# Kernel optimization log

Hardware: AMD Instinct MI355X
Metric: run time of the kernel (lower is better)

## Reference

```python
import jax, jax.numpy as jnp
import numpy as np

N, DIN, H, NCLS = 1024, 128, 64, 40
NEG = -1e30  # stand-in for -inf in masked max (grad-safe)


def _linw(k, fan_in, fan_out):
    s = 1.0 / np.sqrt(fan_in)
    return jax.random.uniform(k, (fan_in, fan_out), jnp.float32, -s, s)


def setup_inputs() -> dict:
    key = jax.random.key(0)
    ks = jax.random.split(key, 10)
    x = jax.random.normal(ks[0], (N, DIN), jnp.float32)
    A = jax.random.bernoulli(ks[1], 0.05, (N, N))  # bool adjacency
    D2 = 2 * H  # layer output width (concat self || neigh)
    return {
        "x": x, "A": A,
        # layer 1 (in=DIN)
        "Wp1": _linw(ks[2], DIN, DIN), "bp1": jnp.zeros((DIN,), jnp.float32),
        "Ws1": _linw(ks[3], DIN, H),   "bs1": jnp.zeros((H,), jnp.float32),
        "Wn1": _linw(ks[4], DIN, H),   "bn1": jnp.zeros((H,), jnp.float32),
        # layer 2 (in=2*H)
        "Wp2": _linw(ks[5], D2, D2),   "bp2": jnp.zeros((D2,), jnp.float32),
        "Ws2": _linw(ks[6], D2, H),    "bs2": jnp.zeros((H,), jnp.float32),
        "Wn2": _linw(ks[7], D2, H),    "bn2": jnp.zeros((H,), jnp.float32),
        # head
        "Wh": _linw(ks[8], D2, NCLS),  "bh": jnp.zeros((NCLS,), jnp.float32),
    }


def _sage_layer(x, A, Wp, bp, Ws, bs, Wn, bn):
    # maxpool aggregator: relu(Linear_pool(x_u)), elementwise max over neighbors u of v
    pooled = jax.nn.relu(x @ Wp + bp)                                  # [N, Din]
    agg = jnp.max(jnp.where(A[:, :, None], pooled[None, :, :], NEG), axis=1)  # [N, Din]
    agg = jnp.where(agg <= NEG * 0.5, 0.0, agg)                        # isolated nodes -> 0
    # out_channels = 2*hidden: concat(self transform, neighbor transform)
    return jnp.concatenate([x @ Ws + bs, agg @ Wn + bn], axis=-1)      # [N, 2H]


def _block(x, A, Wp, bp, Ws, bs, Wn, bn):
    h = jax.nn.relu(_sage_layer(x, A, Wp, bp, Ws, bs, Wn, bn))
    nrm = jnp.maximum(jnp.linalg.norm(h, axis=-1, keepdims=True), 1e-12)
    return h / nrm


def reference(x, A, Wp1, bp1, Ws1, bs1, Wn1, bn1,
              Wp2, bp2, Ws2, bs2, Wn2, bn2, Wh, bh):
    h = _block(x, A, Wp1, bp1, Ws1, bs1, Wn1, bn1)
    h = _block(h, A, Wp2, bp2, Ws2, bs2, Wn2, bn2)
    return h @ Wh + bh  # [N, n_classes]
```

## Files before the change

kernel.cpp:

```cpp
#include <hip/hip_runtime.h>

#define NN 1024

__global__ __launch_bounds__(384) void lin_first(
    const float* __restrict__ X, const float* __restrict__ Wp,
    const float* __restrict__ bp, const float* __restrict__ Ws,
    const float* __restrict__ bs, float* __restrict__ pooled,
    float* __restrict__ sbuf)
{
    __shared__ float xL[4][128];
    __shared__ float lp[2][4][192];
    const int v0 = blockIdx.x * 4;
    const int tid = threadIdx.x;
    for (int i = tid; i < 512; i += 384) xL[i >> 7][i & 127] = X[v0 * 128 + i];
    __syncthreads();
    {
        const int kh = (tid >= 192) ? 1 : 0;
        const int j = tid - kh * 192;
        const float* w; int ld;
        if (j < 128) { w = Wp + j;         ld = 128; }
        else         { w = Ws + (j - 128); ld = 64;  }
        float a0 = 0.f, a1 = 0.f, a2 = 0.f, a3 = 0.f;
        const int k0 = kh * 64;
        #pragma unroll 4
        for (int k = 0; k < 64; ++k) {
            const float wv = w[(k0 + k) * ld];
            a0 += xL[0][k0 + k] * wv;  a1 += xL[1][k0 + k] * wv;
            a2 += xL[2][k0 + k] * wv;  a3 += xL[3][k0 + k] * wv;
        }
        lp[kh][0][j] = a0; lp[kh][1][j] = a1; lp[kh][2][j] = a2; lp[kh][3][j] = a3;
    }
    __syncthreads();
    if (tid < 192) {
        #pragma unroll
        for (int r = 0; r < 4; ++r) {
            const float t = lp[0][r][tid] + lp[1][r][tid];
            if (tid < 128) pooled[(v0 + r) * 128 + tid] = fmaxf(t + bp[tid], 0.f);
            else           sbuf[(v0 + r) * 64 + (tid - 128)] = t + bs[tid - 128];
        }
    }
}

template <int MODE>
__global__ __launch_bounds__(512) void agg_kernel(
    const int* __restrict__ A, const float* __restrict__ pooled,
    const float* __restrict__ sbuf,
    const float* __restrict__ Wn, const float* __restrict__ bn,
    const float* __restrict__ Wp2, const float* __restrict__ bp2,
    const float* __restrict__ Ws2, const float* __restrict__ bs2,
    float* __restrict__ out_pooled, float* __restrict__ out_s,
    float* __restrict__ outh)
{
    __shared__ unsigned long long masks[16];
    __shared__ int pfx[16];
    __shared__ int cntS;
    __shared__ int nbr[NN];
    __shared__ float part[4][128];
    __shared__ float aggL[128];
    __shared__ float wpart[4][64];
    __shared__ float hL[128];
    __shared__ float lpart[2][192];
    __shared__ float red[2];

    const int v    = blockIdx.x;
    const int tid  = threadIdx.x;
    const int lane = tid & 63;
    const int wv   = tid >> 6;

    const int* Arow = A + v * NN;
    #pragma unroll
    for (int i = 0; i < 2; ++i) {
        const int c = wv * 2 + i;
        const unsigned long long m = __ballot(Arow[c * 64 + lane] != 0);
        if (lane == 0) masks[c] = m;
    }
    __syncthreads();
    if (tid == 0) {
        int off = 0;
        #pragma unroll
        for (int c = 0; c < 16; ++c) { pfx[c] = off; off += __popcll(masks[c]); }
        cntS = off;
    }
    __syncthreads();
    #pragma unroll
    for (int i = 0; i < 2; ++i) {
        const int c = wv * 2 + i;
        const unsigned long long m = masks[c];
        if ((m >> lane) & 1ull) {
            const int pos = pfx[c] + __popcll(m & ((1ull << lane) - 1ull));
            nbr[pos] = c * 64 + lane;
        }
    }
    __syncthreads();
    const int n = cntS;

    const int d    = tid & 127;
    const int team = tid >> 7;
    float a0 = -1e30f, a1 = -1e30f, a2 = -1e30f, a3 = -1e30f;
    int p = team;
    for (; p + 12 < n; p += 16) {
        a0 = fmaxf(a0, pooled[nbr[p]      * 128 + d]);
        a1 = fmaxf(a1, pooled[nbr[p + 4]  * 128 + d]);
        a2 = fmaxf(a2, pooled[nbr[p + 8]  * 128 + d]);
        a3 = fmaxf(a3, pooled[nbr[p + 12] * 128 + d]);
    }
    for (; p < n; p += 4) a0 = fmaxf(a0, pooled[nbr[p] * 128 + d]);
    part[team][d] = fmaxf(fmaxf(a0, a1), fmaxf(a2, a3));
    __syncthreads();

    if (team == 0) {
        const float m = fmaxf(fmaxf(part[0][d], part[1][d]),
                              fmaxf(part[2][d], part[3][d]));
        aggL[d] = (m <= -5e29f) ? 0.f : m;
    }
    __syncthreads();

    if (d >= 64) {
        const int j = d - 64;
        const float* w = Wn + j;
        const int k0 = team * 32;
        float pv = 0.f;
        #pragma unroll 8
        for (int k = 0; k < 32; ++k) pv += aggL[k0 + k] * w[(k0 + k) * 64];
        wpart[team][j] = pv;
    }
    __syncthreads();

    float val = 0.f;
    if (tid < 128) {
        if (d < 64) val = sbuf[v * 64 + d];
        else {
            const int j = d - 64;
            val = bn[j] + wpart[0][j] + wpart[1][j] + wpart[2][j] + wpart[3][j];
        }
        val = fmaxf(val, 0.f);
        float ss = val * val;
        #pragma unroll
        for (int off = 32; off >= 1; off >>= 1) ss += __shfl_xor(ss, off, 64);
        if ((tid & 63) == 0) red[tid >> 6] = ss;
    }
    __syncthreads();
    if (tid < 128) {
        const float nrm = fmaxf(sqrtf(red[0] + red[1]), 1e-12f);
        hL[tid] = val / nrm;
    }
    __syncthreads();

    if (MODE == 0) {
        if (tid < 384) {
            const int kh = (tid >= 192) ? 1 : 0;
            const int j  = tid - kh * 192;
            const float* w; int ld;
            if (j < 128) { w = Wp2 + j;         ld = 128; }
            else         { w = Ws2 + (j - 128); ld = 64;  }
            float a = 0.f;
            const int k0 = kh * 64;
            #pragma unroll 4
            for (int k = 0; k < 64; ++k) a += hL[k0 + k] * w[(k0 + k) * ld];
            lpart[kh][j] = a;
        }
        __syncthreads();
        if (tid < 192) {
            const float r = lpart[0][tid] + lpart[1][tid];
            if (tid < 128) out_pooled[v * 128 + tid] = fmaxf(r + bp2[tid], 0.f);
            else           out_s[v * 64 + (tid - 128)] = r + bs2[tid - 128];
        }
    } else {
        if (tid < 64 || (tid >= 256 && tid < 320)) {
            const int kh = (tid >= 256) ? 1 : 0;
            const int j  = tid - kh * 256;
            if (j < 40) {
                float a = 0.f;
                const int k0 = kh * 64;
                #pragma unroll 4
                for (int k = 0; k < 64; ++k) a += hL[k0 + k] * Wp2[(k0 + k) * 40 + j];
                lpart[kh][j] = a;
            }
        }
        __syncthreads();
        if (tid < 40) outh[v * 40 + tid] = bp2[tid] + lpart[0][tid] + lpart[1][tid];
    }
}

extern "C" void kernel_launch(void* const* d_in, const int* in_sizes, int n_in,
                              void* d_out, int out_size, void* d_ws, size_t ws_size,
                              hipStream_t stream) {
    const float* x   = (const float*)d_in[0];
    const int*   A   = (const int*)  d_in[1];
    const float* Wp1 = (const float*)d_in[2];
    const float* bp1 = (const float*)d_in[3];
    const float* Ws1 = (const float*)d_in[4];
    const float* bs1 = (const float*)d_in[5];
    const float* Wn1 = (const float*)d_in[6];
    const float* bn1 = (const float*)d_in[7];
    const float* Wp2 = (const float*)d_in[8];
    const float* bp2 = (const float*)d_in[9];
    const float* Ws2 = (const float*)d_in[10];
    const float* bs2 = (const float*)d_in[11];
    const float* Wn2 = (const float*)d_in[12];
    const float* bn2 = (const float*)d_in[13];
    const float* Wh  = (const float*)d_in[14];
    const float* bh  = (const float*)d_in[15];
    float* out = (float*)d_out;

    char* ws = (char*)d_ws;
    float* pooled1 = (float*)(ws);
    float* s1      = (float*)(ws + (512u << 10));
    float* pooled2 = (float*)(ws + (768u << 10));
    float* s2      = (float*)(ws + (1280u << 10));

    lin_first<<<NN / 4, 384, 0, stream>>>(x, Wp1, bp1, Ws1, bs1, pooled1, s1);
    agg_kernel<0><<<NN, 512, 0, stream>>>(A, pooled1, s1, Wn1, bn1,
                                          Wp2, bp2, Ws2, bs2,
                                          pooled2, s2, nullptr);
    agg_kernel<1><<<NN, 512, 0, stream>>>(A, pooled2, s2, Wn2, bn2,
                                          Wh, bh, nullptr, nullptr,
                                          nullptr, nullptr, out);
}
```

Measured before the change: 28.85 us.

## Fuse three launches into one persistent kernel with grid-wide barriers

Replaces the three separate launches (first linear, two aggregation layers) with a single persistent kernel of 256 blocks, each handling 4 nodes, separated by software grid barriers built on atomics. The neighbor lists are built once per block and reused for both layers, and the self-transform results stay in shared memory instead of going through global buffers. The aim is to remove launch gaps and the duplicated adjacency scan. In exchange it depends on all 256 blocks being resident at once, adds barrier spin cost and a memset, and gives each block more serial work with less parallelism per node.

```diff
diff --git a/kernel.cpp b/kernel.cpp
--- a/kernel.cpp
+++ b/kernel.cpp
@@ -1,32 +1,67 @@
 #include <hip/hip_runtime.h>
 
-#define NN 1024
-
-__global__ __launch_bounds__(384) void lin_first(
-    const float* __restrict__ X, const float* __restrict__ Wp,
-    const float* __restrict__ bp, const float* __restrict__ Ws,
-    const float* __restrict__ bs, float* __restrict__ pooled,
-    float* __restrict__ sbuf)
-{
-    __shared__ float xL[4][128];
-    __shared__ float lp[2][4][192];
-    const int v0 = blockIdx.x * 4;
-    const int tid = threadIdx.x;
-    for (int i = tid; i < 512; i += 384) xL[i >> 7][i & 127] = X[v0 * 128 + i];
-    __syncthreads();
-    {
+#define NN   1024
+#define NBLK 256
+
+struct SharedState {
+    float xL[4][128];
+    float s1L[4][64];
+    float s2L[4][64];
+    float aggL[4][128];
+    float hL[4][128];
+    float lp[2][4][192];
+    float redL[4][2];
+    unsigned long long masksL[4][16];
+    int pfxL[4][16];
+    int cntL[4];
+    int nbrL[4][NN];
+};
+
+__device__ __forceinline__ void gbar(int* cnt, int* gen) {
+    __syncthreads();
+    if (threadIdx.x == 0) {
+        const int g = __hip_atomic_load(gen, __ATOMIC_RELAXED,
+                                        __HIP_MEMORY_SCOPE_AGENT);
+        __threadfence();
+        if (__hip_atomic_fetch_add(cnt, 1, __ATOMIC_ACQ_REL,
+                                   __HIP_MEMORY_SCOPE_AGENT) == NBLK - 1) {
+            __hip_atomic_store(cnt, 0, __ATOMIC_RELAXED,
+                               __HIP_MEMORY_SCOPE_AGENT);
+            __hip_atomic_fetch_add(gen, 1, __ATOMIC_RELEASE,
+                                   __HIP_MEMORY_SCOPE_AGENT);
+        } else {
+            int spins = 0;
+            while (__hip_atomic_load(gen, __ATOMIC_ACQUIRE,
+                                     __HIP_MEMORY_SCOPE_AGENT) == g) {
+                __builtin_amdgcn_s_sleep(1);
+                if (++spins > 10000000) break;
+            }
+        }
+        __threadfence();
+    }
+    __syncthreads();
+}
+
+__device__ __forceinline__ void lin_block(
+    const float (&in)[4][128],
+    const float* __restrict__ Wp, const float* __restrict__ bp,
+    const float* __restrict__ Ws, const float* __restrict__ bs,
+    float* __restrict__ pooledG, float (&sL)[4][64],
+    float (&lp)[2][4][192], int v0, int tid)
+{
+    if (tid < 384) {
         const int kh = (tid >= 192) ? 1 : 0;
         const int j = tid - kh * 192;
         const float* w; int ld;
         if (j < 128) { w = Wp + j;         ld = 128; }
         else         { w = Ws + (j - 128); ld = 64;  }
+        const int k0 = kh * 64;
         float a0 = 0.f, a1 = 0.f, a2 = 0.f, a3 = 0.f;
-        const int k0 = kh * 64;
         #pragma unroll 4
         for (int k = 0; k < 64; ++k) {
             const float wv = w[(k0 + k) * ld];
-            a0 += xL[0][k0 + k] * wv;  a1 += xL[1][k0 + k] * wv;
-            a2 += xL[2][k0 + k] * wv;  a3 += xL[3][k0 + k] * wv;
+            a0 += in[0][k0 + k] * wv;  a1 += in[1][k0 + k] * wv;
+            a2 += in[2][k0 + k] * wv;  a3 += in[3][k0 + k] * wv;
         }
         lp[kh][0][j] = a0; lp[kh][1][j] = a1; lp[kh][2][j] = a2; lp[kh][3][j] = a3;
     }
@@ -35,150 +70,151 @@
         #pragma unroll
         for (int r = 0; r < 4; ++r) {
             const float t = lp[0][r][tid] + lp[1][r][tid];
-            if (tid < 128) pooled[(v0 + r) * 128 + tid] = fmaxf(t + bp[tid], 0.f);
-            else           sbuf[(v0 + r) * 64 + (tid - 128)] = t + bs[tid - 128];
-        }
-    }
-}
-
-template <int MODE>
-__global__ __launch_bounds__(512) void agg_kernel(
-    const int* __restrict__ A, const float* __restrict__ pooled,
-    const float* __restrict__ sbuf,
+            if (tid < 128) pooledG[(v0 + r) * 128 + tid] = fmaxf(t + bp[tid], 0.f);
+            else           sL[r][tid - 128] = t + bs[tid - 128];
+        }
+    }
+    __syncthreads();
+}
+
+__device__ __forceinline__ void gather_rows(
+    const float* __restrict__ src, const int (&nbrL)[4][NN],
+    const int (&cntL)[4], float (&aggL)[4][128], int tid)
+{
+    const int d = tid & 127, r = tid >> 7;
+    const int n = cntL[r];
+    const int* nb = nbrL[r];
+    float a0 = -1e30f, a1 = -1e30f, a2 = -1e30f, a3 = -1e30f;
+    int p = 0;
+    for (; p + 3 < n; p += 4) {
+        a0 = fmaxf(a0, src[nb[p]     * 128 + d]);
+        a1 = fmaxf(a1, src[nb[p + 1] * 128 + d]);
+        a2 = fmaxf(a2, src[nb[p + 2] * 128 + d]);
+        a3 = fmaxf(a3, src[nb[p + 3] * 128 + d]);
+    }
+    for (; p < n; ++p) a0 = fmaxf(a0, src[nb[p] * 128 + d]);
+    const float m = fmaxf(fmaxf(a0, a1), fmaxf(a2, a3));
+    aggL[r][d] = (m <= -5e29f) ? 0.f : m;
+    __syncthreads();
+}
+
+__device__ __forceinline__ void wn_norm(
     const float* __restrict__ Wn, const float* __restrict__ bn,
+    const float (&aggL)[4][128], const float (&sL)[4][64],
+    float (&lp)[2][4][192], float (&redL)[4][2], float (&hL)[4][128],
+    int tid)
+{
+    {
+        const int j  = tid & 63;
+        const int r  = (tid >> 6) & 3;
+        const int kh = tid >> 8;
+        const int k0 = kh * 64;
+        float a = 0.f;
+        #pragma unroll 4
+        for (int k = 0; k < 64; ++k) a += aggL[r][k0 + k] * Wn[(k0 + k) * 64 + j];
+        lp[kh][r][j] = a;
+    }
+    __syncthreads();
+    const int d = tid & 127, r = tid >> 7;
+    float val = (d < 64) ? sL[r][d]
+                         : (bn[d - 64] + lp[0][r][d - 64] + lp[1][r][d - 64]);
+    val = fmaxf(val, 0.f);
+    float ss = val * val;
+    #pragma unroll
+    for (int off = 32; off >= 1; off >>= 1) ss += __shfl_xor(ss, off, 64);
+    if ((tid & 63) == 0) redL[r][(tid >> 6) & 1] = ss;
+    __syncthreads();
+    const float nrm = fmaxf(sqrtf(redL[r][0] + redL[r][1]), 1e-12f);
+    hL[r][d] = val / nrm;
+    __syncthreads();
+}
+
+__global__ __launch_bounds__(512, 4) void fused_sage(
+    const float* __restrict__ x, const int* __restrict__ A,
+    const float* __restrict__ Wp1, const float* __restrict__ bp1,
+    const float* __restrict__ Ws1, const float* __restrict__ bs1,
+    const float* __restrict__ Wn1, const float* __restrict__ bn1,
     const float* __restrict__ Wp2, const float* __restrict__ bp2,
     const float* __restrict__ Ws2, const float* __restrict__ bs2,
-    float* __restrict__ out_pooled, float* __restrict__ out_s,
-    float* __restrict__ outh)
-{
-    __shared__ unsigned long long masks[16];
-    __shared__ int pfx[16];
-    __shared__ int cntS;
-    __shared__ int nbr[NN];
-    __shared__ float part[4][128];
-    __shared__ float aggL[128];
-    __shared__ float wpart[4][64];
-    __shared__ float hL[128];
-    __shared__ float lpart[2][192];
-    __shared__ float red[2];
-
-    const int v    = blockIdx.x;
+    const float* __restrict__ Wn2, const float* __restrict__ bn2,
+    const float* __restrict__ Wh, const float* __restrict__ bh,
+    float* __restrict__ out, float* __restrict__ pooled1,
+    float* __restrict__ pooled2, int* __restrict__ bar)
+{
+    __shared__ SharedState S;
     const int tid  = threadIdx.x;
     const int lane = tid & 63;
     const int wv   = tid >> 6;
-
-    const int* Arow = A + v * NN;
-    #pragma unroll
-    for (int i = 0; i < 2; ++i) {
-        const int c = wv * 2 + i;
-        const unsigned long long m = __ballot(Arow[c * 64 + lane] != 0);
-        if (lane == 0) masks[c] = m;
-    }
-    __syncthreads();
-    if (tid == 0) {
+    const int v0   = blockIdx.x * 4;
+    int* bcnt = bar;
+    int* bgen = bar + 32;
+
+    S.xL[tid >> 7][tid & 127] = x[v0 * 128 + tid];
+    __syncthreads();
+    lin_block(S.xL, Wp1, bp1, Ws1, bs1, pooled1, S.s1L, S.lp, v0, tid);
+
+    {
+        const int r = wv >> 1;
+        const int* Arow = A + (v0 + r) * NN;
+        #pragma unroll
+        for (int c8 = 0; c8 < 8; ++c8) {
+            const int c = (wv & 1) * 8 + c8;
+            const unsigned long long m = __ballot(Arow[c * 64 + lane] != 0);
+            if (lane == 0) S.masksL[r][c] = m;
+        }
+    }
+    __syncthreads();
+    if (tid < 4) {
         int off = 0;
         #pragma unroll
-        for (int c = 0; c < 16; ++c) { pfx[c] = off; off += __popcll(masks[c]); }
-        cntS = off;
-    }
-    __syncthreads();
-    #pragma unroll
-    for (int i = 0; i < 2; ++i) {
-        const int c = wv * 2 + i;
-        const unsigned long long m = masks[c];
-        if ((m >> lane) & 1ull) {
-            const int pos = pfx[c] + __popcll(m & ((1ull << lane) - 1ull));
-            nbr[pos] = c * 64 + lane;
-        }
-    }
-    __syncthreads();
-    const int n = cntS;
-
-    const int d    = tid & 127;
-    const int team = tid >> 7;
-    float a0 = -1e30f, a1 = -1e30f, a2 = -1e30f, a3 = -1e30f;
-    int p = team;
-    for (; p + 12 < n; p += 16) {
-        a0 = fmaxf(a0, pooled[nbr[p]      * 128 + d]);
-        a1 = fmaxf(a1, pooled[nbr[p + 4]  * 128 + d]);
-        a2 = fmaxf(a2, pooled[nbr[p + 8]  * 128 + d]);
-        a3 = fmaxf(a3, pooled[nbr[p + 12] * 128 + d]);
-    }
-    for (; p < n; p += 4) a0 = fmaxf(a0, pooled[nbr[p] * 128 + d]);
-    part[team][d] = fmaxf(fmaxf(a0, a1), fmaxf(a2, a3));
-    __syncthreads();
-
-    if (team == 0) {
-        const float m = fmaxf(fmaxf(part[0][d], part[1][d]),
-                              fmaxf(part[2][d], part[3][d]));
-        aggL[d] = (m <= -5e29f) ? 0.f : m;
-    }
-    __syncthreads();
-
-    if (d >= 64) {
-        const int j = d - 64;
-        const float* w = Wn + j;
-        const int k0 = team * 32;
-        float pv = 0.f;
-        #pragma unroll 8
-        for (int k = 0; k < 32; ++k) pv += aggL[k0 + k] * w[(k0 + k) * 64];
-        wpart[team][j] = pv;
-    }
-    __syncthreads();
-
-    float val = 0.f;
-    if (tid < 128) {
-        if (d < 64) val = sbuf[v * 64 + d];
-        else {
-            const int j = d - 64;
-            val = bn[j] + wpart[0][j] + wpart[1][j] + wpart[2][j] + wpart[3][j];
-        }
-        val = fmaxf(val, 0.f);
-        float ss = val * val;
-        #pragma unroll
-        for (int off = 32; off >= 1; off >>= 1) ss += __shfl_xor(ss, off, 64);
-        if ((tid & 63) == 0) red[tid >> 6] = ss;
-    }
-    __syncthreads();
-    if (tid < 128) {
-        const float nrm = fmaxf(sqrtf(red[0] + red[1]), 1e-12f);
-        hL[tid] = val / nrm;
-    }
-    __syncthreads();
-
-    if (MODE == 0) {
-        if (tid < 384) {
-            const int kh = (tid >= 192) ? 1 : 0;
-            const int j  = tid - kh * 192;
-            const float* w; int ld;
-            if (j < 128) { w = Wp2 + j;         ld = 128; }
-            else         { w = Ws2 + (j - 128); ld = 64;  }
-            float a = 0.f;
-            const int k0 = kh * 64;
-            #pragma unroll 4
-            for (int k = 0; k < 64; ++k) a += hL[k0 + k] * w[(k0 + k) * ld];
-            lpart[kh][j] = a;
-        }
-        __syncthreads();
-        if (tid < 192) {
-            const float r = lpart[0][tid] + lpart[1][tid];
-            if (tid < 128) out_pooled[v * 128 + tid] = fmaxf(r + bp2[tid], 0.f);
-            else           out_s[v * 64 + (tid - 128)] = r + bs2[tid - 128];
-        }
-    } else {
-        if (tid < 64 || (tid >= 256 && tid < 320)) {
-            const int kh = (tid >= 256) ? 1 : 0;
-            const int j  = tid - kh * 256;
-            if (j < 40) {
-                float a = 0.f;
-                const int k0 = kh * 64;
-                #pragma unroll 4
-                for (int k = 0; k < 64; ++k) a += hL[k0 + k] * Wp2[(k0 + k) * 40 + j];
-                lpart[kh][j] = a;
+        for (int c = 0; c < 16; ++c) {
+            S.pfxL[tid][c] = off;
+            off += __popcll(S.masksL[tid][c]);
+        }
+        S.cntL[tid] = off;
+    }
+    __syncthreads();
+    {
+        const int r = wv >> 1;
+        #pragma unroll
+        for (int c8 = 0; c8 < 8; ++c8) {
+            const int c = (wv & 1) * 8 + c8;
+            const unsigned long long m = S.masksL[r][c];
+            if ((m >> lane) & 1ull) {
+                const int pos = S.pfxL[r][c] +
+                                __popcll(m & ((1ull << lane) - 1ull));
+                S.nbrL[r][pos] = c * 64 + lane;
             }
         }
-        __syncthreads();
-        if (tid < 40) outh[v * 40 + tid] = bp2[tid] + lpart[0][tid] + lpart[1][tid];
+    }
+
+    gbar(bcnt, bgen);
+
+    gather_rows(pooled1, S.nbrL, S.cntL, S.aggL, tid);
+    wn_norm(Wn1, bn1, S.aggL, S.s1L, S.lp, S.redL, S.hL, tid);
+    lin_block(S.hL, Wp2, bp2, Ws2, bs2, pooled2, S.s2L, S.lp, v0, tid);
+
+    gbar(bcnt, bgen);
+
+    gather_rows(pooled2, S.nbrL, S.cntL, S.aggL, tid);
+    wn_norm(Wn2, bn2, S.aggL, S.s2L, S.lp, S.redL, S.hL, tid);
+
+    if (tid < 320) {
+        const int kh  = (tid >= 160) ? 1 : 0;
+        const int idx = tid - kh * 160;
+        const int r   = idx / 40;
+        const int j   = idx - r * 40;
+        const int k0  = kh * 64;
+        float a = 0.f;
+        #pragma unroll 4
+        for (int k = 0; k < 64; ++k) a += S.hL[r][k0 + k] * Wh[(k0 + k) * 40 + j];
+        S.lp[kh][r][j] = a;
+    }
+    __syncthreads();
+    if (tid < 160) {
+        const int r = tid / 40;
+        const int j = tid - r * 40;
+        out[(v0 + r) * 40 + j] = bh[j] + S.lp[0][r][j] + S.lp[1][r][j];
     }
 }
 
@@ -205,15 +241,13 @@
 
     char* ws = (char*)d_ws;
     float* pooled1 = (float*)(ws);
-    float* s1      = (float*)(ws + (512u << 10));
-    float* pooled2 = (float*)(ws + (768u << 10));
-    float* s2      = (float*)(ws + (1280u << 10));
-
-    lin_first<<<NN / 4, 384, 0, stream>>>(x, Wp1, bp1, Ws1, bs1, pooled1, s1);
-    agg_kernel<0><<<NN, 512, 0, stream>>>(A, pooled1, s1, Wn1, bn1,
-                                          Wp2, bp2, Ws2, bs2,
-                                          pooled2, s2, nullptr);
-    agg_kernel<1><<<NN, 512, 0, stream>>>(A, pooled2, s2, Wn2, bn2,
-                                          Wh, bh, nullptr, nullptr,
-                                          nullptr, nullptr, out);
-}
+    float* pooled2 = (float*)(ws + (512u << 10));
+    int*   bar     = (int*)  (ws + (1024u << 10));
+
+    hipMemsetAsync(bar, 0, 256, stream);
+
+    fused_sage<<<dim3(NBLK), dim3(512), 0, stream>>>(
+        x, A, Wp1, bp1, Ws1, bs1, Wn1, bn1,
+        Wp2, bp2, Ws2, bs2, Wn2, bn2, Wh, bh,
+        out, pooled1, pooled2, bar);
+}
```

Result: slower. 82.39 us (+185.6%).

## Build neighbor lists once in first kernel and reuse in both aggregation layers

Applied to the files above, without the earlier changes.

Moves the adjacency compaction (ballot, prefix sum, scatter) out of both aggregation kernels into the first linear kernel, which writes compacted neighbor lists and counts to global workspace. Each aggregation kernel then loads only its row's neighbor indices instead of reading the full 4 KB adjacency row and doing two extra barriers. This removes a duplicate read of the 4 MB adjacency matrix. The cost is the global write and read of the neighbor lists and a heavier first kernel.

```diff
diff --git a/kernel.cpp b/kernel.cpp
--- a/kernel.cpp
+++ b/kernel.cpp
@@ -2,35 +2,63 @@
 
 #define NN 1024
 
-__global__ __launch_bounds__(384) void lin_first(
+__global__ __launch_bounds__(512) void lin_build(
     const float* __restrict__ X, const float* __restrict__ Wp,
     const float* __restrict__ bp, const float* __restrict__ Ws,
-    const float* __restrict__ bs, float* __restrict__ pooled,
-    float* __restrict__ sbuf)
+    const float* __restrict__ bs, const int* __restrict__ A,
+    float* __restrict__ pooled, float* __restrict__ sbuf,
+    int* __restrict__ nbrG, int* __restrict__ cntG)
 {
     __shared__ float xL[4][128];
     __shared__ float lp[2][4][192];
-    const int v0 = blockIdx.x * 4;
-    const int tid = threadIdx.x;
-    for (int i = tid; i < 512; i += 384) xL[i >> 7][i & 127] = X[v0 * 128 + i];
-    __syncthreads();
-    {
+    __shared__ unsigned long long masksL[4][16];
+    __shared__ int pfxL[4][16];
+
+    const int tid  = threadIdx.x;
+    const int lane = tid & 63;
+    const int wv   = tid >> 6;
+    const int v0   = blockIdx.x * 4;
+
+    xL[tid >> 7][tid & 127] = X[v0 * 128 + tid];
+    __syncthreads();
+
+    if (tid < 384) {
         const int kh = (tid >= 192) ? 1 : 0;
         const int j = tid - kh * 192;
         const float* w; int ld;
         if (j < 128) { w = Wp + j;         ld = 128; }
         else         { w = Ws + (j - 128); ld = 64;  }
+        const int k0 = kh * 64;
         float a0 = 0.f, a1 = 0.f, a2 = 0.f, a3 = 0.f;
-        const int k0 = kh * 64;
         #pragma unroll 4
         for (int k = 0; k < 64; ++k) {
-            const float wv = w[(k0 + k) * ld];
-            a0 += xL[0][k0 + k] * wv;  a1 += xL[1][k0 + k] * wv;
-            a2 += xL[2][k0 + k] * wv;  a3 += xL[3][k0 + k] * wv;
+            const float wvv = w[(k0 + k) * ld];
+            a0 += xL[0][k0 + k] * wvv;  a1 += xL[1][k0 + k] * wvv;
+            a2 += xL[2][k0 + k] * wvv;  a3 += xL[3][k0 + k] * wvv;
         }
         lp[kh][0][j] = a0; lp[kh][1][j] = a1; lp[kh][2][j] = a2; lp[kh][3][j] = a3;
     }
-    __syncthreads();
+    {
+        const int r = wv >> 1;
+        const int* Arow = A + (v0 + r) * NN;
+        #pragma unroll
+        for (int c8 = 0; c8 < 8; ++c8) {
+            const int c = (wv & 1) * 8 + c8;
+            const unsigned long long m = __ballot(Arow[c * 64 + lane] != 0);
+            if (lane == 0) masksL[r][c] = m;
+        }
+    }
+    __syncthreads();
+
+    if (tid < 4) {
+        int off = 0;
+        #pragma unroll
+        for (int c = 0; c < 16; ++c) {
+            pfxL[tid][c] = off;
+            off += __popcll(masksL[tid][c]);
+        }
+        cntG[v0 + tid] = off;
+    }
     if (tid < 192) {
         #pragma unroll
         for (int r = 0; r < 4; ++r) {
@@ -39,22 +67,33 @@
             else           sbuf[(v0 + r) * 64 + (tid - 128)] = t + bs[tid - 128];
         }
     }
+    __syncthreads();
+
+    {
+        const int r = wv >> 1;
+        #pragma unroll
+        for (int c8 = 0; c8 < 8; ++c8) {
+            const int c = (wv & 1) * 8 + c8;
+            const unsigned long long m = masksL[r][c];
+            if ((m >> lane) & 1ull) {
+                const int pos = pfxL[r][c] + __popcll(m & ((1ull << lane) - 1ull));
+                nbrG[(v0 + r) * NN + pos] = c * 64 + lane;
+            }
+        }
+    }
 }
 
 template <int MODE>
 __global__ __launch_bounds__(512) void agg_kernel(
-    const int* __restrict__ A, const float* __restrict__ pooled,
-    const float* __restrict__ sbuf,
+    const int* __restrict__ nbrG, const int* __restrict__ cntG,
+    const float* __restrict__ pooled, const float* __restrict__ sbuf,
     const float* __restrict__ Wn, const float* __restrict__ bn,
     const float* __restrict__ Wp2, const float* __restrict__ bp2,
     const float* __restrict__ Ws2, const float* __restrict__ bs2,
     float* __restrict__ out_pooled, float* __restrict__ out_s,
     float* __restrict__ outh)
 {
-    __shared__ unsigned long long masks[16];
-    __shared__ int pfx[16];
-    __shared__ int cntS;
-    __shared__ int nbr[NN];
+    __shared__ int   nbr[NN];
     __shared__ float part[4][128];
     __shared__ float aggL[128];
     __shared__ float wpart[4][64];
@@ -62,37 +101,12 @@
     __shared__ float lpart[2][192];
     __shared__ float red[2];
 
-    const int v    = blockIdx.x;
-    const int tid  = threadIdx.x;
-    const int lane = tid & 63;
-    const int wv   = tid >> 6;
-
-    const int* Arow = A + v * NN;
-    #pragma unroll
-    for (int i = 0; i < 2; ++i) {
-        const int c = wv * 2 + i;
-        const unsigned long long m = __ballot(Arow[c * 64 + lane] != 0);
-        if (lane == 0) masks[c] = m;
-    }
-    __syncthreads();
-    if (tid == 0) {
-        int off = 0;
-        #pragma unroll
-        for (int c = 0; c < 16; ++c) { pfx[c] = off; off += __popcll(masks[c]); }
-        cntS = off;
-    }
-    __syncthreads();
-    #pragma unroll
-    for (int i = 0; i < 2; ++i) {
-        const int c = wv * 2 + i;
-        const unsigned long long m = masks[c];
-        if ((m >> lane) & 1ull) {
-            const int pos = pfx[c] + __popcll(m & ((1ull << lane) - 1ull));
-            nbr[pos] = c * 64 + lane;
-        }
-    }
-    __syncthreads();
-    const int n = cntS;
+    const int v   = blockIdx.x;
+    const int tid = threadIdx.x;
+
+    const int n = cntG[v];
+    for (int i = tid; i < n; i += 512) nbr[i] = nbrG[v * NN + i];
+    __syncthreads();
 
     const int d    = tid & 127;
     const int team = tid >> 7;
@@ -208,12 +222,15 @@
     float* s1      = (float*)(ws + (512u << 10));
     float* pooled2 = (float*)(ws + (768u << 10));
     float* s2      = (float*)(ws + (1280u << 10));
-
-    lin_first<<<NN / 4, 384, 0, stream>>>(x, Wp1, bp1, Ws1, bs1, pooled1, s1);
-    agg_kernel<0><<<NN, 512, 0, stream>>>(A, pooled1, s1, Wn1, bn1,
+    int*   nbrG    = (int*)  (ws + (1536u << 10));
+    int*   cntG    = (int*)  (ws + (5632u << 10));
+
+    lin_build<<<NN / 4, 512, 0, stream>>>(x, Wp1, bp1, Ws1, bs1, A,
+                                          pooled1, s1, nbrG, cntG);
+    agg_kernel<0><<<NN, 512, 0, stream>>>(nbrG, cntG, pooled1, s1, Wn1, bn1,
                                           Wp2, bp2, Ws2, bs2,
                                           pooled2, s2, nullptr);
-    agg_kernel<1><<<NN, 512, 0, stream>>>(A, pooled2, s2, Wn2, bn2,
+    agg_kernel<1><<<NN, 512, 0, stream>>>(nbrG, cntG, pooled2, s2, Wn2, bn2,
                                           Wh, bh, nullptr, nullptr,
                                           nullptr, nullptr, out);
 }
```

After: 29.71 us. +3.0%, slower.
